# Kernel optimization log

Hardware: AMD Instinct MI355X
Metric: run time of the kernel (lower is better)

The kernel has to match this reference:

```python
import jax, jax.numpy as jnp
import numpy as np

BN_EPS = 1e-5

def _ste_sign(x):
    # forward: sign in {-1,+1}; backward: clipped straight-through (grad 1 on [-1,1])
    s = jnp.where(x >= 0, 1.0, -1.0).astype(x.dtype)
    c = jnp.clip(x, -1.0, 1.0)
    return c + jax.lax.stop_gradient(s - c)

def setup_inputs() -> dict:
    key = jax.random.key(0)
    ks = jax.random.split(key, 8)
    N, C, H, W = 32, 256, 56, 56
    x = jax.random.normal(ks[0], (N, C, H, W), dtype=jnp.float32)
    bias0 = jax.random.normal(ks[1], (C,), dtype=jnp.float32) * 0.1
    w = jax.random.normal(ks[2], (C, C, 1, 1), dtype=jnp.float32) * 0.05
    gamma = jnp.ones((C,), dtype=jnp.float32)
    beta = jnp.zeros((C,), dtype=jnp.float32)
    bias1 = jax.random.normal(ks[3], (C,), dtype=jnp.float32) * 0.1
    alpha = jnp.full((C,), 0.25, dtype=jnp.float32)  # PReLU init
    bias2 = jax.random.normal(ks[4], (C,), dtype=jnp.float32) * 0.1
    return {"x": x, "bias0": bias0, "w": w, "gamma": gamma, "beta": beta,
            "bias1": bias1, "alpha": alpha, "bias2": bias2}

def reference(x, bias0, w, gamma, beta, bias1, alpha, bias2):
    ch = lambda v: v[None, :, None, None]
    # move0: learnable per-channel bias
    out = x + ch(bias0)
    # binary activation: sign (STE)
    out = _ste_sign(out)
    # binarized 1x1 conv: w_bin = mean(|w|) per out-channel * sign(w)
    scale = jnp.mean(jnp.abs(w), axis=(1, 2, 3))              # [O]
    wb = scale[:, None] * _ste_sign(w[:, :, 0, 0])            # [O, C]
    out = jnp.einsum('nchw,oc->nohw', out, wb)                # 1x1 conv
    # bn1: batch statistics (training-mode math)
    mu = jnp.mean(out, axis=(0, 2, 3), keepdims=True)
    var = jnp.var(out, axis=(0, 2, 3), keepdims=True)
    out = ch(gamma) * (out - mu) * jax.lax.rsqrt(var + BN_EPS) + ch(beta)
    # residual add (downsample is None)
    out = out + x
    # move1 -> PReLU -> move2
    out = out + ch(bias1)
    out = jnp.where(out > 0, out, ch(alpha) * out)
    out = out + ch(bias2)
    return out
```

## Files before the change

### kernel.cpp

```cpp
#include <hip/hip_runtime.h>
#include <stdint.h>

typedef unsigned long long u64;
typedef unsigned int u32;

constexpr int kC  = 256;
constexpr int kHW = 3136;
constexpr int kN  = 32;
constexpr int kP  = kN * kHW;
constexpr int kPosPk = 64;
constexpr int kBlkPk = kP / kPosPk;
constexpr int kPosSt = 128;
constexpr int kBlkSt = kP / kPosSt;

constexpr size_t OFF_T     = 0;
constexpr size_t OFF_SCALE = 8192;
constexpr size_t OFF_SUMD  = 9216;
constexpr size_t OFF_SUMD2 = 11264;
constexpr size_t OFF_S     = 13312;

struct alignas(16) U64x2 { u64 x, y; };

__global__ __launch_bounds__(256) void pack_kernel(
    const float* __restrict__ x, const float* __restrict__ bias0,
    const float* __restrict__ w, char* __restrict__ ws) {
  int t = threadIdx.x;
  int b = blockIdx.x;

  if (b < 16) {
    u64*   T     = (u64*)(ws + OFF_T);
    float* scale = (float*)(ws + OFF_SCALE);
    int kk = t >> 6, ln = t & 63;
    if (b == 0) {
      ((u64*)(ws + OFF_SUMD))[t]  = 0ull;
      ((u64*)(ws + OFF_SUMD2))[t] = 0ull;
    }
    __shared__ float part[4][16];
#pragma unroll
    for (int i = 0; i < 16; ++i) {
      int o = b * 16 + i;
      float v = w[o * kC + kk * 64 + ln];
      u64 m = __ballot(v >= 0.0f);
      float a = fabsf(v);
#pragma unroll
      for (int s = 32; s > 0; s >>= 1) a += __shfl_xor(a, s, 64);
      if (ln == 0) { T[kk * 256 + o] = m; part[kk][i] = a; }
    }
    __syncthreads();
    if (t < 16) {
      int o = b * 16 + t;
      scale[o] = (part[0][t] + part[1][t] + part[2][t] + part[3][t]) * (1.0f / 256.0f);
    }
  }

  int k    = __builtin_amdgcn_readfirstlane(t >> 6);
  int lane = t & 63;
  u32 p  = (u32)b * (u32)kPosPk + (u32)lane;
  u32 n  = p / kHW;
  u32 hw = p - n * kHW;
  const float* xp = x + (size_t)n * kC * kHW + (size_t)(k * 64) * kHW + hw;
  const float* bp = bias0 + k * 64;

  u64 m = 0;
#pragma unroll 32
  for (int i = 0; i < 64; ++i) {
    float v = __builtin_nontemporal_load(xp + (size_t)i * kHW) + bp[i];
    m |= (u64)(v >= 0.0f) << i;
  }
  u64* S = (u64*)(ws + OFF_S);
  S[(size_t)k * kP + p] = m;
}

__global__ __launch_bounds__(256) void stats_kernel(char* __restrict__ ws) {
  int o = threadIdx.x;
  const u64* T = (const u64*)(ws + OFF_T);
  u64 t0 = T[o], t1 = T[256 + o], t2 = T[512 + o], t3 = T[768 + o];
  const u64* S = (const u64*)(ws + OFF_S);
  u32 pb = blockIdx.x * (u32)kPosSt;

  int summ = 0, summ2 = 0;
#pragma unroll 8
  for (int j = 0; j < kPosSt; j += 2) {
    u32 p = pb + j;
    U64x2 a0 = *(const U64x2*)&S[p];
    U64x2 a1 = *(const U64x2*)&S[kP + p];
    U64x2 a2 = *(const U64x2*)&S[2 * kP + p];
    U64x2 a3 = *(const U64x2*)&S[3 * kP + p];
    int ka = __popcll(a0.x ^ t0) + __popcll(a1.x ^ t1) +
             __popcll(a2.x ^ t2) + __popcll(a3.x ^ t3);
    int kb = __popcll(a0.y ^ t0) + __popcll(a1.y ^ t1) +
             __popcll(a2.y ^ t2) + __popcll(a3.y ^ t3);
    int ma = 128 - ka, mb = 128 - kb;
    summ  += ma + mb;
    summ2 += ma * ma + mb * mb;
  }
  atomicAdd((u64*)(ws + OFF_SUMD) + o,  (u64)(long long)(2 * summ));
  atomicAdd((u64*)(ws + OFF_SUMD2) + o, (u64)(long long)(4 * summ2));
}

__global__ __launch_bounds__(256) void finalize_kernel(
    const float* __restrict__ x, const float* __restrict__ gamma,
    const float* __restrict__ beta, const float* __restrict__ bias1,
    const float* __restrict__ alpha, const float* __restrict__ bias2,
    const char* __restrict__ ws, float* __restrict__ out) {
  __shared__ u64    ldsT[256][4];
  __shared__ float4 ldsC[256];

  int t = threadIdx.x;
  {
    const u64* T = (const u64*)(ws + OFF_T);
#pragma unroll
    for (int q = 0; q < 4; ++q) ldsT[t][q] = T[q * 256 + t];

    const float*     scale = (const float*)(ws + OFF_SCALE);
    const long long* sumd  = (const long long*)(ws + OFF_SUMD);
    const long long* sumd2 = (const long long*)(ws + OFF_SUMD2);
    double inv  = 1.0 / (double)kP;
    double md   = (double)sumd[t] * inv;
    double e2   = (double)sumd2[t] * inv;
    double vard = e2 - md * md;
    float sc  = scale[t];
    float mu  = sc * (float)md;
    float var = sc * sc * (float)vard;
    float rs  = rsqrtf(var + 1e-5f);
    float g   = gamma[t];
    float cA  = g * rs * sc;
    float cB  = beta[t] - g * rs * mu + bias1[t];
    ldsC[t] = make_float4(2.0f * cA, cB, alpha[t], bias2[t]);
  }
  __syncthreads();

  int k    = __builtin_amdgcn_readfirstlane(t >> 6);
  int lane = t & 63;
  u32 p  = blockIdx.x * (u32)kPosPk + (u32)lane;
  u32 n  = p / kHW;
  u32 hw = p - n * kHW;

  const u64* S = (const u64*)(ws + OFF_S);
  u64 s0 = S[p];
  u64 s1 = S[kP + p];
  u64 s2 = S[2 * kP + p];
  u64 s3 = S[3 * kP + p];

  const float* xp = x   + (size_t)n * kC * kHW + (size_t)(k * 64) * kHW + hw;
  float*       op = out + (size_t)n * kC * kHW + (size_t)(k * 64) * kHW + hw;

#pragma unroll 8
  for (int i = 0; i < 64; ++i) {
    int o = k * 64 + i;
    u64 w0 = ldsT[o][0], w1 = ldsT[o][1], w2 = ldsT[o][2], w3 = ldsT[o][3];
    int kx = __popcll(s0 ^ w0) + __popcll(s1 ^ w1) +
             __popcll(s2 ^ w2) + __popcll(s3 ^ w3);
    float4 cc = ldsC[o];
    float xv = __builtin_nontemporal_load(xp + (size_t)i * kHW);
    float u  = fmaf(cc.x, (float)(128 - kx), cc.y) + xv;
    float r  = u > 0.0f ? u : cc.z * u;
    __builtin_nontemporal_store(r + cc.w, op + (size_t)i * kHW);
  }
}

extern "C" void kernel_launch(void* const* d_in, const int* in_sizes, int n_in,
                              void* d_out, int out_size, void* d_ws, size_t ws_size,
                              hipStream_t stream) {
  const float* x     = (const float*)d_in[0];
  const float* bias0 = (const float*)d_in[1];
  const float* w     = (const float*)d_in[2];
  const float* gamma = (const float*)d_in[3];
  const float* beta  = (const float*)d_in[4];
  const float* bias1 = (const float*)d_in[5];
  const float* alpha = (const float*)d_in[6];
  const float* bias2 = (const float*)d_in[7];
  float* out = (float*)d_out;
  char*  ws  = (char*)d_ws;

  hipLaunchKernelGGL(pack_kernel, dim3(kBlkPk), dim3(256), 0, stream,
                     x, bias0, w, ws);
  hipLaunchKernelGGL(stats_kernel, dim3(kBlkSt), dim3(256), 0, stream, ws);
  hipLaunchKernelGGL(finalize_kernel, dim3(kBlkPk), dim3(256), 0, stream,
                     x, gamma, beta, bias1, alpha, bias2, ws, out);
}
```

Measured before the change: 242.3 us.

## Fuse sign-packing with BN stats and process two positions per lane

Weight binarization moves into a small separate prep kernel. Activation sign-packing and the popcount statistics are fused into one kernel: each block packs 128 positions, syncs, then computes per-channel sums from those freshly written bits, likely still in cache. Both the packing and finalize kernels now handle two adjacent positions per lane with 8-byte vector loads and stores, which halves the block count and widens memory accesses. The trade-off is that the nontemporal hint on the x loads in packing is dropped, and the stats phase reads global memory written by other waves of the same block after only a __syncthreads.

Result: slower. 266.3 us (+9.9%).

```diff
diff --git a/kernel.cpp b/kernel.cpp
--- a/kernel.cpp
+++ b/kernel.cpp
@@ -3,15 +3,14 @@
 
 typedef unsigned long long u64;
 typedef unsigned int u32;
+typedef float f32x2 __attribute__((ext_vector_type(2)));
 
 constexpr int kC  = 256;
 constexpr int kHW = 3136;
 constexpr int kN  = 32;
 constexpr int kP  = kN * kHW;
-constexpr int kPosPk = 64;
-constexpr int kBlkPk = kP / kPosPk;
-constexpr int kPosSt = 128;
-constexpr int kBlkSt = kP / kPosSt;
+constexpr int kPos = 128;
+constexpr int kBlk = kP / kPos;
 
 constexpr size_t OFF_T     = 0;
 constexpr size_t OFF_SCALE = 8192;
@@ -21,71 +20,72 @@
 
 struct alignas(16) U64x2 { u64 x, y; };
 
-__global__ __launch_bounds__(256) void pack_kernel(
-    const float* __restrict__ x, const float* __restrict__ bias0,
+__global__ __launch_bounds__(256) void prep_kernel(
     const float* __restrict__ w, char* __restrict__ ws) {
   int t = threadIdx.x;
   int b = blockIdx.x;
+  u64*   T     = (u64*)(ws + OFF_T);
+  float* scale = (float*)(ws + OFF_SCALE);
+  int kk = t >> 6, ln = t & 63;
+  if (b == 0) {
+    ((u64*)(ws + OFF_SUMD))[t]  = 0ull;
+    ((u64*)(ws + OFF_SUMD2))[t] = 0ull;
+  }
+  __shared__ float part[4][16];
+#pragma unroll
+  for (int i = 0; i < 16; ++i) {
+    int o = b * 16 + i;
+    float v = w[o * kC + kk * 64 + ln];
+    u64 m = __ballot(v >= 0.0f);
+    float a = fabsf(v);
+#pragma unroll
+    for (int s = 32; s > 0; s >>= 1) a += __shfl_xor(a, s, 64);
+    if (ln == 0) { T[kk * 256 + o] = m; part[kk][i] = a; }
+  }
+  __syncthreads();
+  if (t < 16) {
+    int o = b * 16 + t;
+    scale[o] = (part[0][t] + part[1][t] + part[2][t] + part[3][t]) * (1.0f / 256.0f);
+  }
+}
 
-  if (b < 16) {
-    u64*   T     = (u64*)(ws + OFF_T);
-    float* scale = (float*)(ws + OFF_SCALE);
-    int kk = t >> 6, ln = t & 63;
-    if (b == 0) {
-      ((u64*)(ws + OFF_SUMD))[t]  = 0ull;
-      ((u64*)(ws + OFF_SUMD2))[t] = 0ull;
-    }
-    __shared__ float part[4][16];
-#pragma unroll
-    for (int i = 0; i < 16; ++i) {
-      int o = b * 16 + i;
-      float v = w[o * kC + kk * 64 + ln];
-      u64 m = __ballot(v >= 0.0f);
-      float a = fabsf(v);
-#pragma unroll
-      for (int s = 32; s > 0; s >>= 1) a += __shfl_xor(a, s, 64);
-      if (ln == 0) { T[kk * 256 + o] = m; part[kk][i] = a; }
-    }
-    __syncthreads();
-    if (t < 16) {
-      int o = b * 16 + t;
-      scale[o] = (part[0][t] + part[1][t] + part[2][t] + part[3][t]) * (1.0f / 256.0f);
-    }
-  }
-
+__global__ __launch_bounds__(256) void pack_stats_kernel(
+    const float* __restrict__ x, const float* __restrict__ bias0,
+    char* __restrict__ ws) {
+  int t = threadIdx.x;
   int k    = __builtin_amdgcn_readfirstlane(t >> 6);
   int lane = t & 63;
-  u32 p  = (u32)b * (u32)kPosPk + (u32)lane;
+  u32 pb = blockIdx.x * (u32)kPos;
+  u32 p  = pb + 2u * (u32)lane;
   u32 n  = p / kHW;
   u32 hw = p - n * kHW;
   const float* xp = x + (size_t)n * kC * kHW + (size_t)(k * 64) * kHW + hw;
   const float* bp = bias0 + k * 64;
 
-  u64 m = 0;
-#pragma unroll 32
+  u64 m0 = 0, m1 = 0;
+#pragma unroll 8
   for (int i = 0; i < 64; ++i) {
-    float v = __builtin_nontemporal_load(xp + (size_t)i * kHW) + bp[i];
-    m |= (u64)(v >= 0.0f) << i;
+    f32x2 v = *(const f32x2*)(xp + (size_t)i * kHW);
+    float bi = bp[i];
+    m0 |= (u64)(v.x + bi >= 0.0f) << i;
+    m1 |= (u64)(v.y + bi >= 0.0f) << i;
   }
   u64* S = (u64*)(ws + OFF_S);
-  S[(size_t)k * kP + p] = m;
-}
+  U64x2 st; st.x = m0; st.y = m1;
+  *(U64x2*)&S[(size_t)k * kP + p] = st;
 
-__global__ __launch_bounds__(256) void stats_kernel(char* __restrict__ ws) {
-  int o = threadIdx.x;
+  __syncthreads();
+
   const u64* T = (const u64*)(ws + OFF_T);
-  u64 t0 = T[o], t1 = T[256 + o], t2 = T[512 + o], t3 = T[768 + o];
-  const u64* S = (const u64*)(ws + OFF_S);
-  u32 pb = blockIdx.x * (u32)kPosSt;
-
+  u64 t0 = T[t], t1 = T[256 + t], t2 = T[512 + t], t3 = T[768 + t];
   int summ = 0, summ2 = 0;
 #pragma unroll 8
-  for (int j = 0; j < kPosSt; j += 2) {
-    u32 p = pb + j;
-    U64x2 a0 = *(const U64x2*)&S[p];
-    U64x2 a1 = *(const U64x2*)&S[kP + p];
-    U64x2 a2 = *(const U64x2*)&S[2 * kP + p];
-    U64x2 a3 = *(const U64x2*)&S[3 * kP + p];
+  for (int j = 0; j < kPos; j += 2) {
+    u32 q = pb + j;
+    U64x2 a0 = *(const U64x2*)&S[q];
+    U64x2 a1 = *(const U64x2*)&S[kP + q];
+    U64x2 a2 = *(const U64x2*)&S[2 * kP + q];
+    U64x2 a3 = *(const U64x2*)&S[3 * kP + q];
     int ka = __popcll(a0.x ^ t0) + __popcll(a1.x ^ t1) +
              __popcll(a2.x ^ t2) + __popcll(a3.x ^ t3);
     int kb = __popcll(a0.y ^ t0) + __popcll(a1.y ^ t1) +
@@ -94,8 +94,8 @@
     summ  += ma + mb;
     summ2 += ma * ma + mb * mb;
   }
-  atomicAdd((u64*)(ws + OFF_SUMD) + o,  (u64)(long long)(2 * summ));
-  atomicAdd((u64*)(ws + OFF_SUMD2) + o, (u64)(long long)(4 * summ2));
+  atomicAdd((u64*)(ws + OFF_SUMD) + t,  (u64)(long long)(2 * summ));
+  atomicAdd((u64*)(ws + OFF_SUMD2) + t, (u64)(long long)(4 * summ2));
 }
 
 __global__ __launch_bounds__(256) void finalize_kernel(
@@ -132,15 +132,15 @@
 
   int k    = __builtin_amdgcn_readfirstlane(t >> 6);
   int lane = t & 63;
-  u32 p  = blockIdx.x * (u32)kPosPk + (u32)lane;
+  u32 p  = blockIdx.x * (u32)kPos + 2u * (u32)lane;
   u32 n  = p / kHW;
   u32 hw = p - n * kHW;
 
   const u64* S = (const u64*)(ws + OFF_S);
-  u64 s0 = S[p];
-  u64 s1 = S[kP + p];
-  u64 s2 = S[2 * kP + p];
-  u64 s3 = S[3 * kP + p];
+  U64x2 s0 = *(const U64x2*)&S[p];
+  U64x2 s1 = *(const U64x2*)&S[kP + p];
+  U64x2 s2 = *(const U64x2*)&S[2 * kP + p];
+  U64x2 s3 = *(const U64x2*)&S[3 * kP + p];
 
   const float* xp = x   + (size_t)n * kC * kHW + (size_t)(k * 64) * kHW + hw;
   float*       op = out + (size_t)n * kC * kHW + (size_t)(k * 64) * kHW + hw;
@@ -149,13 +149,18 @@
   for (int i = 0; i < 64; ++i) {
     int o = k * 64 + i;
     u64 w0 = ldsT[o][0], w1 = ldsT[o][1], w2 = ldsT[o][2], w3 = ldsT[o][3];
-    int kx = __popcll(s0 ^ w0) + __popcll(s1 ^ w1) +
-             __popcll(s2 ^ w2) + __popcll(s3 ^ w3);
     float4 cc = ldsC[o];
-    float xv = __builtin_nontemporal_load(xp + (size_t)i * kHW);
-    float u  = fmaf(cc.x, (float)(128 - kx), cc.y) + xv;
-    float r  = u > 0.0f ? u : cc.z * u;
-    __builtin_nontemporal_store(r + cc.w, op + (size_t)i * kHW);
+    f32x2 xv = *(const f32x2*)(xp + (size_t)i * kHW);
+    int ka = __popcll(s0.x ^ w0) + __popcll(s1.x ^ w1) +
+             __popcll(s2.x ^ w2) + __popcll(s3.x ^ w3);
+    int kb = __popcll(s0.y ^ w0) + __popcll(s1.y ^ w1) +
+             __popcll(s2.y ^ w2) + __popcll(s3.y ^ w3);
+    float ua = fmaf(cc.x, (float)(128 - ka), cc.y) + xv.x;
+    float ub = fmaf(cc.x, (float)(128 - kb), cc.y) + xv.y;
+    f32x2 r;
+    r.x = (ua > 0.0f ? ua : cc.z * ua) + cc.w;
+    r.y = (ub > 0.0f ? ub : cc.z * ub) + cc.w;
+    __builtin_nontemporal_store(r, (f32x2*)(op + (size_t)i * kHW));
   }
 }
 
@@ -173,9 +178,9 @@
   float* out = (float*)d_out;
   char*  ws  = (char*)d_ws;
 
-  hipLaunchKernelGGL(pack_kernel, dim3(kBlkPk), dim3(256), 0, stream,
-                     x, bias0, w, ws);
-  hipLaunchKernelGGL(stats_kernel, dim3(kBlkSt), dim3(256), 0, stream, ws);
-  hipLaunchKernelGGL(finalize_kernel, dim3(kBlkPk), dim3(256), 0, stream,
+  hipLaunchKernelGGL(prep_kernel, dim3(16), dim3(256), 0, stream, w, ws);
+  hipLaunchKernelGGL(pack_stats_kernel, dim3(kBlk), dim3(256), 0, stream,
+                     x, bias0, ws);
+  hipLaunchKernelGGL(finalize_kernel, dim3(kBlk), dim3(256), 0, stream,
                      x, gamma, beta, bias1, alpha, bias2, ws, out);
 }
```

## Replace per-block stats atomics with two-stage partial reduction; split weight prep kernel

Applied to the files above, without the earlier changes.

The stats kernel now writes per-block partial sums to workspace arrays instead of issuing 64-bit atomics from every block (784 blocks x 256 channels). A new 16-block reduce kernel sums 49 rows each and does only 16 atomics per channel. The weight sign-packing and scale computation move out of pack_kernel into a separate prep kernel. This cuts atomic contention at the cost of two extra kernel launches and some extra workspace traffic.

Measured after the change: 246.3 us. About the same (+1.6%).

```diff
diff --git a/kernel.cpp b/kernel.cpp
--- a/kernel.cpp
+++ b/kernel.cpp
@@ -12,47 +12,53 @@
 constexpr int kBlkPk = kP / kPosPk;
 constexpr int kPosSt = 128;
 constexpr int kBlkSt = kP / kPosSt;
+constexpr int kRedBlk = 16;
+constexpr int kRedRows = 49;
 
 constexpr size_t OFF_T     = 0;
 constexpr size_t OFF_SCALE = 8192;
 constexpr size_t OFF_SUMD  = 9216;
 constexpr size_t OFF_SUMD2 = 11264;
 constexpr size_t OFF_S     = 13312;
+constexpr size_t OFF_PS    = 3224576;
+constexpr size_t OFF_PQ    = 4027392;
 
 struct alignas(16) U64x2 { u64 x, y; };
+
+__global__ __launch_bounds__(256) void prep_kernel(
+    const float* __restrict__ w, char* __restrict__ ws) {
+  int t = threadIdx.x;
+  int b = blockIdx.x;
+  u64*   T     = (u64*)(ws + OFF_T);
+  float* scale = (float*)(ws + OFF_SCALE);
+  int kk = t >> 6, ln = t & 63;
+  if (b == 0) {
+    ((u64*)(ws + OFF_SUMD))[t]  = 0ull;
+    ((u64*)(ws + OFF_SUMD2))[t] = 0ull;
+  }
+  __shared__ float part[4][16];
+#pragma unroll
+  for (int i = 0; i < 16; ++i) {
+    int o = b * 16 + i;
+    float v = w[o * kC + kk * 64 + ln];
+    u64 m = __ballot(v >= 0.0f);
+    float a = fabsf(v);
+#pragma unroll
+    for (int s = 32; s > 0; s >>= 1) a += __shfl_xor(a, s, 64);
+    if (ln == 0) { T[kk * 256 + o] = m; part[kk][i] = a; }
+  }
+  __syncthreads();
+  if (t < 16) {
+    int o = b * 16 + t;
+    scale[o] = (part[0][t] + part[1][t] + part[2][t] + part[3][t]) * (1.0f / 256.0f);
+  }
+}
 
 __global__ __launch_bounds__(256) void pack_kernel(
     const float* __restrict__ x, const float* __restrict__ bias0,
-    const float* __restrict__ w, char* __restrict__ ws) {
+    char* __restrict__ ws) {
   int t = threadIdx.x;
   int b = blockIdx.x;
-
-  if (b < 16) {
-    u64*   T     = (u64*)(ws + OFF_T);
-    float* scale = (float*)(ws + OFF_SCALE);
-    int kk = t >> 6, ln = t & 63;
-    if (b == 0) {
-      ((u64*)(ws + OFF_SUMD))[t]  = 0ull;
-      ((u64*)(ws + OFF_SUMD2))[t] = 0ull;
-    }
-    __shared__ float part[4][16];
-#pragma unroll
-    for (int i = 0; i < 16; ++i) {
-      int o = b * 16 + i;
-      float v = w[o * kC + kk * 64 + ln];
-      u64 m = __ballot(v >= 0.0f);
-      float a = fabsf(v);
-#pragma unroll
-      for (int s = 32; s > 0; s >>= 1) a += __shfl_xor(a, s, 64);
-      if (ln == 0) { T[kk * 256 + o] = m; part[kk][i] = a; }
-    }
-    __syncthreads();
-    if (t < 16) {
-      int o = b * 16 + t;
-      scale[o] = (part[0][t] + part[1][t] + part[2][t] + part[3][t]) * (1.0f / 256.0f);
-    }
-  }
-
   int k    = __builtin_amdgcn_readfirstlane(t >> 6);
   int lane = t & 63;
   u32 p  = (u32)b * (u32)kPosPk + (u32)lane;
@@ -94,8 +100,24 @@
     summ  += ma + mb;
     summ2 += ma * ma + mb * mb;
   }
-  atomicAdd((u64*)(ws + OFF_SUMD) + o,  (u64)(long long)(2 * summ));
-  atomicAdd((u64*)(ws + OFF_SUMD2) + o, (u64)(long long)(4 * summ2));
+  ((int*)(ws + OFF_PS))[blockIdx.x * 256 + o] = summ;
+  ((int*)(ws + OFF_PQ))[blockIdx.x * 256 + o] = summ2;
+}
+
+__global__ __launch_bounds__(256) void reduce_kernel(char* __restrict__ ws) {
+  int t = threadIdx.x;
+  int b = blockIdx.x;
+  const int* PS = (const int*)(ws + OFF_PS);
+  const int* PQ = (const int*)(ws + OFF_PQ);
+  long long s = 0, q = 0;
+#pragma unroll 7
+  for (int r = 0; r < kRedRows; ++r) {
+    int row = b * kRedRows + r;
+    s += PS[row * 256 + t];
+    q += PQ[row * 256 + t];
+  }
+  atomicAdd((u64*)(ws + OFF_SUMD) + t,  (u64)(long long)(2 * s));
+  atomicAdd((u64*)(ws + OFF_SUMD2) + t, (u64)(long long)(4 * q));
 }
 
 __global__ __launch_bounds__(256) void finalize_kernel(
@@ -173,9 +195,11 @@
   float* out = (float*)d_out;
   char*  ws  = (char*)d_ws;
 
+  hipLaunchKernelGGL(prep_kernel, dim3(16), dim3(256), 0, stream, w, ws);
   hipLaunchKernelGGL(pack_kernel, dim3(kBlkPk), dim3(256), 0, stream,
-                     x, bias0, w, ws);
+                     x, bias0, ws);
   hipLaunchKernelGGL(stats_kernel, dim3(kBlkSt), dim3(256), 0, stream, ws);
+  hipLaunchKernelGGL(reduce_kernel, dim3(kRedBlk), dim3(256), 0, stream, ws);
   hipLaunchKernelGGL(finalize_kernel, dim3(kBlkPk), dim3(256), 0, stream,
                      x, gamma, beta, bias1, alpha, bias2, ws, out);
 }
```
